# Performance work log

Hardware: AMD Instinct MI355X
Metric: run time of the kernel (lower is better)

Reference implementation:

```python
import jax, jax.numpy as jnp
import numpy as np

V, E, H, L, B = 50000, 300, 128, 32, 8


def setup_inputs() -> dict:
    key = jax.random.key(0)
    ks = jax.random.split(key, 12)
    s = 0.05
    d = {}
    d["premise"] = jax.random.randint(ks[0], (B, L), 0, V)
    d["hypothesis"] = jax.random.randint(ks[1], (B, L), 0, V)
    d["emb"] = jax.random.normal(ks[2], (V, E), jnp.float32) * s
    d["W_ih"] = jax.random.normal(ks[3], (8 * H, 2 * E), jnp.float32) * s
    d["b_ih"] = jnp.zeros((8 * H,), jnp.float32)
    d["W_hh"] = jax.random.normal(ks[4], (8 * H, 2 * H), jnp.float32) * s
    d["b_hh"] = jnp.zeros((8 * H,), jnp.float32)
    d["W_ch"] = jax.random.normal(ks[5], (H, 2 * H), jnp.float32) * s
    d["b_ch"] = jnp.zeros((H,), jnp.float32)
    d["W_cc"] = jax.random.normal(ks[6], (H, 2 * H), jnp.float32) * s
    d["b_cc"] = jnp.zeros((H,), jnp.float32)
    d["W1"] = jax.random.normal(ks[7], (H, H), jnp.float32) * s
    d["b1"] = jnp.zeros((H,), jnp.float32)
    d["W2"] = jax.random.normal(ks[8], (H, H), jnp.float32) * s
    d["b2"] = jnp.zeros((H,), jnp.float32)
    d["W3"] = jax.random.normal(ks[9], (3, H), jnp.float32) * s
    d["b3"] = jnp.zeros((3,), jnp.float32)
    return d


def _lstm_cell(x, h, c, W_ih, b_ih, W_hh, b_hh):
    # PyTorch LSTMCell gate order: i, f, g, o
    g = x @ W_ih.T + b_ih + h @ W_hh.T + b_hh
    i, f, gg, o = jnp.split(g, 4, axis=-1)
    c_new = jax.nn.sigmoid(f) * c + jax.nn.sigmoid(i) * jnp.tanh(gg)
    h_new = jax.nn.sigmoid(o) * jnp.tanh(c_new)
    return h_new, c_new


def reference(premise, hypothesis, emb, W_ih, b_ih, W_hh, b_hh,
              W_ch, b_ch, W_cc, b_cc, W1, b1, W2, b2, W3, b3):
    p = emb[premise]      # [B, L, E]
    hyp = emb[hypothesis]  # [B, L, E]
    Bn, Ln, En = p.shape
    Hn = W_ch.shape[0]
    p_t = jnp.swapaxes(p, 0, 1)    # [L, B, E]
    hyp_t = jnp.swapaxes(hyp, 0, 1)
    z = jnp.zeros((Bn, Hn), p.dtype)

    def row_step(row_carry, p_i):
        h_up, c_up = row_carry  # [L, B, H] from previous row (left deps)

        def col_step(carry, xs):
            h_low, c_low = carry       # [B, H] from previous column (lower deps)
            h_u, c_u, x_hyp = xs       # [B,H], [B,H], [B,E]
            x = jnp.concatenate([p_i, x_hyp], axis=-1)       # [B, 2E]
            h_in = jnp.concatenate([h_u, h_low], axis=-1)    # left then lower -> [B, 2H]
            c_in = jnp.concatenate([c_u, c_low], axis=-1)
            h_o, c_o = _lstm_cell(x, h_in, c_in, W_ih, b_ih, W_hh, b_hh)
            h_n = h_o @ W_ch.T + b_ch  # condense back to [B, H]
            c_n = c_o @ W_cc.T + b_cc
            return (h_n, c_n), (h_n, c_n)

        _, (h_row, c_row) = jax.lax.scan(col_step, (z, z), (h_up, c_up, hyp_t))
        return (h_row, c_row), None

    init = (jnp.zeros((Ln, Bn, Hn), p.dtype), jnp.zeros((Ln, Bn, Hn), p.dtype))
    (h_grid, _), _ = jax.lax.scan(row_step, init, p_t)
    h = h_grid[-1]  # h[L, L] corner state, [B, H]
    h = jax.nn.relu(h @ W1.T + b1)
    h = jax.nn.relu(h @ W2.T + b2)
    return jax.nn.softmax(h @ W3.T + b3, axis=1)
```

## Files before the change

### kernel.cpp

```cpp
#include <hip/hip_runtime.h>
#include <math.h>


typedef _Float16 h2 __attribute__((ext_vector_type(2)));

__device__ __forceinline__ h2 pk_f16(float a, float b) {
    return __builtin_bit_cast(h2, __builtin_amdgcn_cvt_pkrtz(a, b));
}

#define HYP_OFF   0
#define WP_OFF    262144
#define B_OFF     524288
#define INITF_OFF 526336
#define WF_OFF    530432
#define HO_OFF    546816
#define CO_OFF    677888
#define HOF_OFF   940032

#define BASE 0xAAAAAAAAu

__device__ __forceinline__ float sigm(float x) { return 1.f / (1.f + __expf(-x)); }
__device__ __forceinline__ float tanh_fast(float x) { return 1.f - 2.f / (__expf(2.f * x) + 1.f); }

__device__ __forceinline__ unsigned ld_flag(const unsigned* p) {
    return __hip_atomic_load(p, __ATOMIC_RELAXED, __HIP_MEMORY_SCOPE_AGENT);
}
__device__ __forceinline__ void st_flag(unsigned* p, unsigned v) {
    __hip_atomic_store(p, v, __ATOMIC_RELAXED, __HIP_MEMORY_SCOPE_AGENT);
}
__device__ __forceinline__ float ld_f32(const float* p) {
    unsigned u = __hip_atomic_load((const unsigned*)p, __ATOMIC_RELAXED, __HIP_MEMORY_SCOPE_AGENT);
    return __uint_as_float(u);
}
__device__ __forceinline__ void st_f32(float* p, float v) {
    __hip_atomic_store((unsigned*)p, __float_as_uint(v), __ATOMIC_RELAXED, __HIP_MEMORY_SCOPE_AGENT);
}
__device__ __forceinline__ void st_u32(unsigned* p, unsigned v) {
    __hip_atomic_store(p, v, __ATOMIC_RELAXED, __HIP_MEMORY_SCOPE_AGENT);
}
__device__ __forceinline__ unsigned long long ld_u64(const unsigned long long* p) {
    return __hip_atomic_load(p, __ATOMIC_RELAXED, __HIP_MEMORY_SCOPE_AGENT);
}
__device__ __forceinline__ float2 ld_f32x2(const float* p) {
    unsigned long long u = ld_u64((const unsigned long long*)p);
    float2 r; r.x = __uint_as_float((unsigned)u); r.y = __uint_as_float((unsigned)(u >> 32));
    return r;
}
__device__ __forceinline__ void wait_ge(const unsigned* f, unsigned target) {
    long spins = 0;
    while ((ld_flag(f) - BASE) < target) {
        __builtin_amdgcn_s_sleep(1);
        if (++spins > (1L << 22)) break;
    }
}
__device__ __forceinline__ void drain_vmem() {
    asm volatile("s_waitcnt vmcnt(0)" ::: "memory");
}

__global__ void __launch_bounds__(256, 1) grid_lstm_kernel(
    const int* __restrict__ premise, const int* __restrict__ hypothesis,
    const float* __restrict__ emb,
    const float* __restrict__ W_ih, const float* __restrict__ b_ih,
    const float* __restrict__ W_hh, const float* __restrict__ b_hh,
    const float* __restrict__ W_ch, const float* __restrict__ b_ch,
    const float* __restrict__ W_cc, const float* __restrict__ b_cc,
    const float* __restrict__ W1, const float* __restrict__ b1,
    const float* __restrict__ W2, const float* __restrict__ b2,
    const float* __restrict__ W3, const float* __restrict__ b3,
    float* __restrict__ out, float* __restrict__ ws)
{
    __shared__ h2    hAB[2048];
    __shared__ float sCo[2048];
    __shared__ float ppL[1024];
    __shared__ float red[8448];
    __shared__ float red2[2304];

    const int tid = threadIdx.x;
    const int bid = blockIdx.x;
    const int i   = bid & 31;
    const int c   = bid >> 5;

    float*    Hypproj = ws + HYP_OFF;
    unsigned* WP      = (unsigned*)(ws + WP_OFF);
    float*    BU      = ws + B_OFF;
    float*    BL      = ws + B_OFF + 1024;
    unsigned* InitF   = (unsigned*)(ws + INITF_OFF);
    unsigned* WF      = (unsigned*)(ws + WF_OFF);
    unsigned* Ho      = (unsigned*)(ws + HO_OFF);
    float*    Co      = ws + CO_OFF;
    float*    HoF     = ws + HOF_OFF;

    const int tq = tid & 31, ks = tid >> 5;
    const int tl = tid & 31, bb = tid >> 5;

    {
        float* embs = red;
        for (int idx = tid; idx < 4800; idx += 256) {
            int side = idx / 2400, rem = idx - side * 2400;
            int b = rem / 300, e = rem - b * 300;
            const int* toks = side ? hypothesis : premise;
            embs[idx] = emb[(long)toks[b * 32 + i] * 300 + e];
        }
        __syncthreads();
        #pragma unroll 1
        for (int q = 0; q < 4; q++) {
            const int oo = tid + q * 256;
            const int b = oo >> 7, g = oo & 127;
            const int gr = (g >> 5) * 256 + c * 32 + (g & 31);
            float accP = b_ih[gr] + b_hh[gr];
            float accH = 0.f;
            const float* wp = W_ih + (long)gr * 600;
            const float* eP = embs + b * 300;
            const float* eH = embs + 2400 + b * 300;
            for (int e = 0; e < 300; e += 4) {
                float4 w1 = *(const float4*)(wp + e);
                float4 w2v = *(const float4*)(wp + 300 + e);
                float4 p4 = *(const float4*)(eP + e);
                float4 h4 = *(const float4*)(eH + e);
                accP += w1.x * p4.x + w1.y * p4.y + w1.z * p4.z + w1.w * p4.w;
                accH += w2v.x * h4.x + w2v.y * h4.y + w2v.z * h4.z + w2v.w * h4.w;
            }
            st_f32(&Hypproj[i * 8192 + b * 1024 + gr], accH);
            ppL[b * 128 + g] = accP;
        }
        __syncthreads();
    }

    {
        const int tr = tid >> 6, col = (tid & 63) * 4;
        const int r  = bid * 4 + tr;
        float u[4] = {0.f, 0.f, 0.f, 0.f}, l[4] = {0.f, 0.f, 0.f, 0.f};
        const float* whU = W_hh + (long)r * 256;
        const float* whL = whU + 128;
        for (int k = 0; k < 128; k++) {
            const float wu = whU[k], wl = whL[k];
            float4 wc = *(const float4*)(W_ch + (long)k * 256 + col);
            u[0] += wu * wc.x; u[1] += wu * wc.y; u[2] += wu * wc.z; u[3] += wu * wc.w;
            l[0] += wl * wc.x; l[1] += wl * wc.y; l[2] += wl * wc.z; l[3] += wl * wc.w;
        }
        unsigned* wrow = WP + (long)r * 256;
        st_u32(&wrow[col / 2],       __builtin_bit_cast(unsigned, __builtin_amdgcn_cvt_pkrtz(u[0], u[1])));
        st_u32(&wrow[col / 2 + 1],   __builtin_bit_cast(unsigned, __builtin_amdgcn_cvt_pkrtz(u[2], u[3])));
        st_u32(&wrow[128 + col / 2],     __builtin_bit_cast(unsigned, __builtin_amdgcn_cvt_pkrtz(l[0], l[1])));
        st_u32(&wrow[128 + col / 2 + 1], __builtin_bit_cast(unsigned, __builtin_amdgcn_cvt_pkrtz(l[2], l[3])));
        if ((tid & 63) == 0) {
            float su = 0.f, sl = 0.f;
            for (int k = 0; k < 128; k++) { su += whU[k] * b_ch[k]; sl += whL[k] * b_ch[k]; }
            st_f32(&BU[r], su); st_f32(&BL[r], sl);
        }
    }
    drain_vmem();
    __syncthreads();
    if (tid == 0) st_flag(&InitF[bid * 16], BASE + 1u);

    wait_ge(&InitF[tid * 16], 1u);
    __syncthreads();

    h2 w[4][32];
    #pragma unroll
    for (int a = 0; a < 4; a++) {
        const unsigned* src = WP + (long)(a * 256 + c * 32 + tq) * 256 + ks * 32;
        #pragma unroll
        for (int m = 0; m < 16; m++) {
            unsigned long long u2 = ld_u64((const unsigned long long*)(src + m * 2));
            w[a][2 * m]     = __builtin_bit_cast(h2, (unsigned)u2);
            w[a][2 * m + 1] = __builtin_bit_cast(h2, (unsigned)(u2 >> 32));
        }
    }
    float4 w3[8];
    {
        const float* wr = W_cc + (long)((c & 3) * 32 + tq) * 256 + ks * 32;
        #pragma unroll
        for (int m = 0; m < 8; m++) w3[m] = *(const float4*)(wr + m * 4);
    }
    float bUv[4], bLv[4];
    #pragma unroll
    for (int a = 0; a < 4; a++) {
        bUv[a] = ld_f32(&BU[a * 256 + c * 32 + tl]);
        bLv[a] = ld_f32(&BL[a * 256 + c * 32 + tl]);
    }

    #pragma unroll 1
    for (int j = 0; j < 32; j++) {
        const bool upok = (i > 0), lfok = (j > 0);
        const bool cok  = (c < 4) ? upok : lfok;
        const int  jl   = lfok ? (j - 1) : 0;

        {
            const unsigned* fp = nullptr;
            unsigned tgt = 0;
            if (upok && tid < 32) {
                fp = &WF[(((i - 1) * 8 + (tid >> 2)) * 4 + (tid & 3)) * 16];
                tgt = (unsigned)(j + 1);
            } else if (lfok && tid >= 32 && tid < 60) {
                int s = tid - 32;
                int cc = s >> 2;
                cc += (cc >= c) ? 1 : 0;
                fp = &WF[((i * 8 + cc) * 4 + (s & 3)) * 16];
                tgt = (unsigned)j;
            }
            if (fp) wait_ge(fp, tgt);
        }
        __syncthreads();

        const unsigned* HoUp = Ho + (size_t)(((i - 1) & 3) * 32 + j) * 1024;
        const unsigned* HoLf = Ho + (size_t)((i & 3) * 32 + jl) * 1024;
        const float*    CoS  = (c < 4)
            ? Co + (size_t)(((i - 1) & 3) * 32 + j) * 2048
            : Co + (size_t)((i & 3) * 32 + jl) * 2048;
        const int hi = tid >> 7, kk = tid & 127;

        float hyv[4];
        #pragma unroll
        for (int a = 0; a < 4; a++)
            hyv[a] = ld_f32(&Hypproj[j * 8192 + bb * 1024 + a * 256 + c * 32 + tl]);
        unsigned uu[4], ll[4];
        float2   cc2[4];
        #pragma unroll
        for (int r = 0; r < 4; r++)
            uu[r] = upok ? ld_flag(HoUp + (2 * r + hi) * 128 + kk) : 0u;
        #pragma unroll
        for (int r = 0; r < 4; r++)
            ll[r] = lfok ? ld_flag(HoLf + (2 * r + hi) * 128 + kk) : 0u;
        #pragma unroll
        for (int r = 0; r < 4; r++)
            cc2[r] = cok ? ld_f32x2(CoS + (2 * r + hi) * 256 + 2 * kk) : make_float2(0.f, 0.f);
        __builtin_amdgcn_sched_barrier(0);
        #pragma unroll
        for (int r = 0; r < 4; r++) {
            const int b = 2 * r + hi;
            hAB[b * 256 + kk]       = __builtin_bit_cast(h2, uu[r]);
            hAB[b * 256 + 128 + kk] = __builtin_bit_cast(h2, ll[r]);
            sCo[b * 256 + 2 * kk]     = cc2[r].x;
            sCo[b * 256 + 2 * kk + 1] = cc2[r].y;
        }
        __syncthreads();

        float acc[4][8], a3[8];
        #pragma unroll
        for (int a = 0; a < 4; a++)
            #pragma unroll
            for (int b = 0; b < 8; b++) acc[a][b] = 0.f;
        #pragma unroll
        for (int b = 0; b < 8; b++) a3[b] = 0.f;
        #pragma unroll
        for (int b = 0; b < 8; b++) {
            const h2*    hb = hAB + b * 256 + ks * 32;
            const float* cb = sCo + b * 256 + ks * 32;
            #pragma unroll
            for (int m4 = 0; m4 < 8; m4++) {
                uint4 hu = *(const uint4*)(hb + m4 * 4);
                h2 h0 = __builtin_bit_cast(h2, hu.x);
                h2 h1 = __builtin_bit_cast(h2, hu.y);
                h2 h2v = __builtin_bit_cast(h2, hu.z);
                h2 h3 = __builtin_bit_cast(h2, hu.w);
                #pragma unroll
                for (int a = 0; a < 4; a++) {
                    acc[a][b] = __builtin_amdgcn_fdot2(w[a][m4 * 4],     h0,  acc[a][b], false);
                    acc[a][b] = __builtin_amdgcn_fdot2(w[a][m4 * 4 + 1], h1,  acc[a][b], false);
                    acc[a][b] = __builtin_amdgcn_fdot2(w[a][m4 * 4 + 2], h2v, acc[a][b], false);
                    acc[a][b] = __builtin_amdgcn_fdot2(w[a][m4 * 4 + 3], h3,  acc[a][b], false);
                }
                float4 cv = *(const float4*)(cb + m4 * 4);
                a3[b] += w3[m4].x * cv.x + w3[m4].y * cv.y + w3[m4].z * cv.z + w3[m4].w * cv.w;
            }
        }
        #pragma unroll
        for (int a = 0; a < 4; a++)
            #pragma unroll
            for (int b = 0; b < 8; b++) red[tid * 33 + a * 8 + b] = acc[a][b];
        #pragma unroll
        for (int b = 0; b < 8; b++) red2[tid * 9 + b] = a3[b];
        __syncthreads();

        {
            float g4[4];
            #pragma unroll
            for (int a = 0; a < 4; a++) {
                float s = 0.f;
                #pragma unroll
                for (int k = 0; k < 8; k++)
                    s += red[(k * 32 + tl) * 33 + a * 8 + bb];
                s += ppL[bb * 128 + a * 32 + tl] + hyv[a];
                if (upok) s += bUv[a];
                if (lfok) s += bLv[a];
                g4[a] = s;
            }
            float ci = 0.f;
            #pragma unroll
            for (int k = 0; k < 8; k++) ci += red2[(k * 32 + tl) * 9 + bb];
            if (cok) ci += b_cc[(c & 3) * 32 + tl];
            const float cnew = sigm(g4[1]) * ci + sigm(g4[0]) * tanh_fast(g4[2]);
            const float hnew = sigm(g4[3]) * tanh_fast(cnew);

            const int slot = (i & 3) * 32 + j;
            st_f32(&Co[(size_t)slot * 2048 + bb * 256 + c * 32 + tl], cnew);
            const float hOdd = __shfl_xor(hnew, 1);
            if ((tl & 1) == 0)
                st_u32(&Ho[(size_t)slot * 1024 + bb * 128 + c * 16 + (tl >> 1)],
                       __builtin_bit_cast(unsigned, pk_f16(hnew, hOdd)));
            if (i == 31 && j == 31)
                st_f32(&HoF[bb * 256 + c * 32 + tl], hnew);
        }
        drain_vmem();
        if ((tid & 63) == 0)
            st_flag(&WF[((i * 8 + c) * 4 + (tid >> 6)) * 16], BASE + (unsigned)(j + 1));
    }

    if (bid == 31) {
        if (tid < 32)
            wait_ge(&WF[((31 * 8 + (tid >> 2)) * 4 + (tid & 3)) * 16], 32u);
        __syncthreads();
        #pragma unroll
        for (int r = 0; r < 8; r++)
            sCo[r * 256 + tid] = ld_f32(&HoF[r * 256 + tid]);
        __syncthreads();
        #pragma unroll 1
        for (int q = 0; q < 4; q++) {
            const int oo = tid + q * 256;
            const int b = oo >> 7, o = oo & 127;
            float a = b_ch[o];
            const float* wr = W_ch + (long)o * 256;
            const float* x = sCo + b * 256;
            for (int k = 0; k < 256; k += 4) {
                float4 wv = *(const float4*)(wr + k);
                float4 xv = *(const float4*)(x + k);
                a += wv.x * xv.x + wv.y * xv.y + wv.z * xv.z + wv.w * xv.w;
            }
            ppL[b * 128 + o] = a;
        }
        __syncthreads();
        float* m1 = red;
        float* m2 = red + 1024;
        for (int idx = tid; idx < 1024; idx += 256) {
            int b = idx >> 7, o = idx & 127;
            float a = b1[o];
            const float* wr = W1 + o * 128; const float* x = ppL + b * 128;
            for (int k = 0; k < 128; k++) a += wr[k] * x[k];
            m1[idx] = fmaxf(a, 0.f);
        }
        __syncthreads();
        for (int idx = tid; idx < 1024; idx += 256) {
            int b = idx >> 7, o = idx & 127;
            float a = b2[o];
            const float* wr = W2 + o * 128; const float* x = m1 + b * 128;
            for (int k = 0; k < 128; k++) a += wr[k] * x[k];
            m2[idx] = fmaxf(a, 0.f);
        }
        __syncthreads();
        if (tid < 8) {
            const int b = tid;
            float lg[3];
            for (int cc = 0; cc < 3; cc++) {
                float a = b3[cc];
                const float* wr = W3 + cc * 128; const float* x = m2 + b * 128;
                for (int k = 0; k < 128; k++) a += wr[k] * x[k];
                lg[cc] = a;
            }
            float m = fmaxf(lg[0], fmaxf(lg[1], lg[2]));
            float e0 = expf(lg[0] - m), e1 = expf(lg[1] - m), e2 = expf(lg[2] - m);
            float s = e0 + e1 + e2;
            out[b * 3 + 0] = e0 / s;
            out[b * 3 + 1] = e1 / s;
            out[b * 3 + 2] = e2 / s;
        }
    }
}

extern "C" void kernel_launch(void* const* d_in, const int* in_sizes, int n_in,
                              void* d_out, int out_size, void* d_ws, size_t ws_size,
                              hipStream_t stream) {
    const int*   premise    = (const int*)d_in[0];
    const int*   hypothesis = (const int*)d_in[1];
    const float* emb        = (const float*)d_in[2];
    const float* W_ih       = (const float*)d_in[3];
    const float* b_ih       = (const float*)d_in[4];
    const float* W_hh       = (const float*)d_in[5];
    const float* b_hh       = (const float*)d_in[6];
    const float* W_ch       = (const float*)d_in[7];
    const float* b_ch       = (const float*)d_in[8];
    const float* W_cc       = (const float*)d_in[9];
    const float* b_cc       = (const float*)d_in[10];
    const float* W1         = (const float*)d_in[11];
    const float* b1         = (const float*)d_in[12];
    const float* W2         = (const float*)d_in[13];
    const float* b2         = (const float*)d_in[14];
    const float* W3         = (const float*)d_in[15];
    const float* b3         = (const float*)d_in[16];
    float* out = (float*)d_out;
    float* ws  = (float*)d_ws;

    (void)in_sizes; (void)n_in; (void)out_size; (void)ws_size;

    grid_lstm_kernel<<<dim3(256), dim3(256), 0, stream>>>(
        premise, hypothesis, emb, W_ih, b_ih, W_hh, b_hh,
        W_ch, b_ch, W_cc, b_cc, W1, b1, W2, b2, W3, b3, out, ws);
}
```

Baseline: 764.6 us.

## Tag each h/c value with a step id to drop vmem drains before flags

New measurement: 659.6 us. 13.7% less time.

```diff
diff --git a/kernel.cpp b/kernel.cpp
--- a/kernel.cpp
+++ b/kernel.cpp
@@ -3,6 +3,7 @@
 
 
 typedef _Float16 h2 __attribute__((ext_vector_type(2)));
+typedef unsigned long long ull;
 
 __device__ __forceinline__ h2 pk_f16(float a, float b) {
     return __builtin_bit_cast(h2, __builtin_amdgcn_cvt_pkrtz(a, b));
@@ -12,10 +13,10 @@
 #define WP_OFF    262144
 #define B_OFF     524288
 #define INITF_OFF 526336
-#define WF_OFF    530432
-#define HO_OFF    546816
-#define CO_OFF    677888
-#define HOF_OFF   940032
+#define WF_OFF    527360
+#define HOT_OFF   531456
+#define COT_OFF   793600
+#define HOF_OFF   1317888
 
 #define BASE 0xAAAAAAAAu
 
@@ -38,13 +39,11 @@
 __device__ __forceinline__ void st_u32(unsigned* p, unsigned v) {
     __hip_atomic_store(p, v, __ATOMIC_RELAXED, __HIP_MEMORY_SCOPE_AGENT);
 }
-__device__ __forceinline__ unsigned long long ld_u64(const unsigned long long* p) {
+__device__ __forceinline__ ull ld_u64(const ull* p) {
     return __hip_atomic_load(p, __ATOMIC_RELAXED, __HIP_MEMORY_SCOPE_AGENT);
 }
-__device__ __forceinline__ float2 ld_f32x2(const float* p) {
-    unsigned long long u = ld_u64((const unsigned long long*)p);
-    float2 r; r.x = __uint_as_float((unsigned)u); r.y = __uint_as_float((unsigned)(u >> 32));
-    return r;
+__device__ __forceinline__ void st_u64(ull* p, ull v) {
+    __hip_atomic_store(p, v, __ATOMIC_RELAXED, __HIP_MEMORY_SCOPE_AGENT);
 }
 __device__ __forceinline__ void wait_ge(const unsigned* f, unsigned target) {
     long spins = 0;
@@ -86,9 +85,9 @@
     float*    BL      = ws + B_OFF + 1024;
     unsigned* InitF   = (unsigned*)(ws + INITF_OFF);
     unsigned* WF      = (unsigned*)(ws + WF_OFF);
-    unsigned* Ho      = (unsigned*)(ws + HO_OFF);
-    float*    Co      = ws + CO_OFF;
-    float*    HoF     = ws + HOF_OFF;
+    ull*      HoT     = (ull*)(ws + HOT_OFF);
+    ull*      CoT     = (ull*)(ws + COT_OFF);
+    ull*      HoF     = (ull*)(ws + HOF_OFF);
 
     const int tq = tid & 31, ks = tid >> 5;
     const int tl = tid & 31, bb = tid >> 5;
@@ -151,9 +150,9 @@
     }
     drain_vmem();
     __syncthreads();
-    if (tid == 0) st_flag(&InitF[bid * 16], BASE + 1u);
-
-    wait_ge(&InitF[tid * 16], 1u);
+    if (tid == 0) st_flag(&InitF[bid * 4], BASE + 1u);
+
+    wait_ge(&InitF[tid * 4], 1u);
     __syncthreads();
 
     h2 w[4][32];
@@ -162,7 +161,7 @@
         const unsigned* src = WP + (long)(a * 256 + c * 32 + tq) * 256 + ks * 32;
         #pragma unroll
         for (int m = 0; m < 16; m++) {
-            unsigned long long u2 = ld_u64((const unsigned long long*)(src + m * 2));
+            ull u2 = ld_u64((const ull*)(src + m * 2));
             w[a][2 * m]     = __builtin_bit_cast(h2, (unsigned)u2);
             w[a][2 * m + 1] = __builtin_bit_cast(h2, (unsigned)(u2 >> 32));
         }
@@ -186,53 +185,71 @@
         const bool cok  = (c < 4) ? upok : lfok;
         const int  jl   = lfok ? (j - 1) : 0;
 
+        const unsigned upTag = (unsigned)((i - 1) * 32 + j + 1);
+        const unsigned lfTag = (unsigned)(i * 32 + j);
+        const unsigned coTag = (c < 4) ? upTag : lfTag;
+
         {
             const unsigned* fp = nullptr;
             unsigned tgt = 0;
             if (upok && tid < 32) {
-                fp = &WF[(((i - 1) * 8 + (tid >> 2)) * 4 + (tid & 3)) * 16];
+                fp = &WF[(((i - 1) * 8 + (tid >> 2)) * 4 + (tid & 3)) * 4];
                 tgt = (unsigned)(j + 1);
             } else if (lfok && tid >= 32 && tid < 60) {
                 int s = tid - 32;
                 int cc = s >> 2;
                 cc += (cc >= c) ? 1 : 0;
-                fp = &WF[((i * 8 + cc) * 4 + (s & 3)) * 16];
+                fp = &WF[((i * 8 + cc) * 4 + (s & 3)) * 4];
                 tgt = (unsigned)j;
             }
             if (fp) wait_ge(fp, tgt);
         }
         __syncthreads();
 
-        const unsigned* HoUp = Ho + (size_t)(((i - 1) & 3) * 32 + j) * 1024;
-        const unsigned* HoLf = Ho + (size_t)((i & 3) * 32 + jl) * 1024;
-        const float*    CoS  = (c < 4)
-            ? Co + (size_t)(((i - 1) & 3) * 32 + j) * 2048
-            : Co + (size_t)((i & 3) * 32 + jl) * 2048;
+        const ull* HoUpT = HoT + (size_t)(((i - 1) & 3) * 32 + j) * 1024;
+        const ull* HoLfT = HoT + (size_t)((i & 3) * 32 + jl) * 1024;
+        const ull* CoST  = (c < 4)
+            ? CoT + (size_t)(((i - 1) & 3) * 32 + j) * 2048
+            : CoT + (size_t)((i & 3) * 32 + jl) * 2048;
         const int hi = tid >> 7, kk = tid & 127;
 
         float hyv[4];
         #pragma unroll
         for (int a = 0; a < 4; a++)
             hyv[a] = ld_f32(&Hypproj[j * 8192 + bb * 1024 + a * 256 + c * 32 + tl]);
-        unsigned uu[4], ll[4];
-        float2   cc2[4];
-        #pragma unroll
-        for (int r = 0; r < 4; r++)
-            uu[r] = upok ? ld_flag(HoUp + (2 * r + hi) * 128 + kk) : 0u;
-        #pragma unroll
-        for (int r = 0; r < 4; r++)
-            ll[r] = lfok ? ld_flag(HoLf + (2 * r + hi) * 128 + kk) : 0u;
-        #pragma unroll
-        for (int r = 0; r < 4; r++)
-            cc2[r] = cok ? ld_f32x2(CoS + (2 * r + hi) * 256 + 2 * kk) : make_float2(0.f, 0.f);
+
+        ull uv[4] = {0, 0, 0, 0}, lv[4] = {0, 0, 0, 0};
+        ull cv[8] = {0, 0, 0, 0, 0, 0, 0, 0};
+        unsigned pend = (upok ? 0x000Fu : 0u) | (lfok ? 0x00F0u : 0u) | (cok ? 0xFF00u : 0u);
+        long spins = 0;
+        while (pend) {
+            #pragma unroll
+            for (int r = 0; r < 4; r++) {
+                if (pend & (1u << r))        uv[r] = ld_u64(HoUpT + (2 * r + hi) * 128 + kk);
+                if (pend & (0x10u << r))     lv[r] = ld_u64(HoLfT + (2 * r + hi) * 128 + kk);
+                if (pend & (0x100u << 2*r))  cv[2*r]   = ld_u64(CoST + (2 * r + hi) * 256 + 2 * kk);
+                if (pend & (0x200u << 2*r))  cv[2*r+1] = ld_u64(CoST + (2 * r + hi) * 256 + 2 * kk + 1);
+            }
+            #pragma unroll
+            for (int r = 0; r < 4; r++) {
+                if ((pend & (1u << r))       && (unsigned)(uv[r] >> 32) == upTag)      pend &= ~(1u << r);
+                if ((pend & (0x10u << r))    && (unsigned)(lv[r] >> 32) == lfTag)      pend &= ~(0x10u << r);
+                if ((pend & (0x100u << 2*r)) && (unsigned)(cv[2*r] >> 32) == coTag)    pend &= ~(0x100u << 2*r);
+                if ((pend & (0x200u << 2*r)) && (unsigned)(cv[2*r+1] >> 32) == coTag)  pend &= ~(0x200u << 2*r);
+            }
+            if (pend) {
+                __builtin_amdgcn_s_sleep(1);
+                if (++spins > (1L << 22)) break;
+            }
+        }
         __builtin_amdgcn_sched_barrier(0);
         #pragma unroll
         for (int r = 0; r < 4; r++) {
             const int b = 2 * r + hi;
-            hAB[b * 256 + kk]       = __builtin_bit_cast(h2, uu[r]);
-            hAB[b * 256 + 128 + kk] = __builtin_bit_cast(h2, ll[r]);
-            sCo[b * 256 + 2 * kk]     = cc2[r].x;
-            sCo[b * 256 + 2 * kk + 1] = cc2[r].y;
+            hAB[b * 256 + kk]       = __builtin_bit_cast(h2, (unsigned)uv[r]);
+            hAB[b * 256 + 128 + kk] = __builtin_bit_cast(h2, (unsigned)lv[r]);
+            sCo[b * 256 + 2 * kk]     = __uint_as_float((unsigned)cv[2*r]);
+            sCo[b * 256 + 2 * kk + 1] = __uint_as_float((unsigned)cv[2*r+1]);
         }
         __syncthreads();
 
@@ -261,8 +278,8 @@
                     acc[a][b] = __builtin_amdgcn_fdot2(w[a][m4 * 4 + 2], h2v, acc[a][b], false);
                     acc[a][b] = __builtin_amdgcn_fdot2(w[a][m4 * 4 + 3], h3,  acc[a][b], false);
                 }
-                float4 cv = *(const float4*)(cb + m4 * 4);
-                a3[b] += w3[m4].x * cv.x + w3[m4].y * cv.y + w3[m4].z * cv.z + w3[m4].w * cv.w;
+                float4 cv4 = *(const float4*)(cb + m4 * 4);
+                a3[b] += w3[m4].x * cv4.x + w3[m4].y * cv4.y + w3[m4].z * cv4.z + w3[m4].w * cv4.w;
             }
         }
         #pragma unroll
@@ -293,27 +310,50 @@
             const float cnew = sigm(g4[1]) * ci + sigm(g4[0]) * tanh_fast(g4[2]);
             const float hnew = sigm(g4[3]) * tanh_fast(cnew);
 
+            const unsigned myTag = (unsigned)(i * 32 + j + 1);
+            const ull tagHi = ((ull)myTag) << 32;
             const int slot = (i & 3) * 32 + j;
-            st_f32(&Co[(size_t)slot * 2048 + bb * 256 + c * 32 + tl], cnew);
+
+            st_u64(&CoT[(size_t)slot * 2048 + bb * 256 + c * 32 + tl],
+                   tagHi | (ull)__float_as_uint(cnew));
             const float hOdd = __shfl_xor(hnew, 1);
             if ((tl & 1) == 0)
-                st_u32(&Ho[(size_t)slot * 1024 + bb * 128 + c * 16 + (tl >> 1)],
-                       __builtin_bit_cast(unsigned, pk_f16(hnew, hOdd)));
+                st_u64(&HoT[(size_t)slot * 1024 + bb * 128 + c * 16 + (tl >> 1)],
+                       tagHi | (ull)__builtin_bit_cast(unsigned, pk_f16(hnew, hOdd)));
             if (i == 31 && j == 31)
-                st_f32(&HoF[bb * 256 + c * 32 + tl], hnew);
-        }
-        drain_vmem();
+                st_u64(&HoF[bb * 256 + c * 32 + tl],
+                       tagHi | (ull)__float_as_uint(hnew));
+        }
         if ((tid & 63) == 0)
-            st_flag(&WF[((i * 8 + c) * 4 + (tid >> 6)) * 16], BASE + (unsigned)(j + 1));
+            st_flag(&WF[((i * 8 + c) * 4 + (tid >> 6)) * 4], BASE + (unsigned)(j + 1));
     }
 
     if (bid == 31) {
         if (tid < 32)
-            wait_ge(&WF[((31 * 8 + (tid >> 2)) * 4 + (tid & 3)) * 16], 32u);
-        __syncthreads();
-        #pragma unroll
-        for (int r = 0; r < 8; r++)
-            sCo[r * 256 + tid] = ld_f32(&HoF[r * 256 + tid]);
+            wait_ge(&WF[((31 * 8 + (tid >> 2)) * 4 + (tid & 3)) * 4], 32u);
+        __syncthreads();
+        const unsigned fTag = 1024u;
+        float hov[8] = {0.f, 0.f, 0.f, 0.f, 0.f, 0.f, 0.f, 0.f};
+        unsigned pf = 0xFFu;
+        long spins = 0;
+        while (pf) {
+            ull tv[8];
+            #pragma unroll
+            for (int r = 0; r < 8; r++)
+                if (pf & (1u << r)) tv[r] = ld_u64(HoF + r * 256 + tid);
+            #pragma unroll
+            for (int r = 0; r < 8; r++)
+                if ((pf & (1u << r)) && (unsigned)(tv[r] >> 32) == fTag) {
+                    hov[r] = __uint_as_float((unsigned)tv[r]);
+                    pf &= ~(1u << r);
+                }
+            if (pf) {
+                __builtin_amdgcn_s_sleep(1);
+                if (++spins > (1L << 22)) break;
+            }
+        }
+        #pragma unroll
+        for (int r = 0; r < 8; r++) sCo[r * 256 + tid] = hov[r];
         __syncthreads();
         #pragma unroll 1
         for (int q = 0; q < 4; q++) {
```
